# Kernel optimization log

Measured on AMD Instinct MI355X. Metric: run time of the kernel, lower is better.

Reference implementation:

```python
import jax, jax.numpy as jnp
import numpy as np
from jax import lax

T, B, D, H, C, G = 32, 512, 1024, 2048, 10, 16
BETA = 0.95
THRESH = 1.0


def _build_mask(key, out_f, in_f, p_intra=1.0, p_inter=0.15):
    ig, og = in_f // G, out_f // G
    same = (jnp.arange(out_f) // og)[:, None] == (jnp.arange(in_f) // ig)[None, :]
    probs = jnp.where(same, p_intra, p_inter)
    return (jax.random.uniform(key, (out_f, in_f)) < probs).astype(jnp.float32)


def setup_inputs() -> dict:
    key = jax.random.key(0)
    ks = jax.random.split(key, 12)
    def w(k, out_f, in_f):
        return jax.random.normal(k, (out_f, in_f), jnp.float32) * (1.0 / np.sqrt(in_f))
    return {
        'x_seq': jax.random.normal(ks[0], (T, B, D), jnp.float32),
        'w1': w(ks[1], H, D), 'b1': jax.random.normal(ks[2], (H,), jnp.float32) * 0.01,
        'mask1': _build_mask(ks[3], H, D),
        'w2': w(ks[4], H, H), 'b2': jax.random.normal(ks[5], (H,), jnp.float32) * 0.01,
        'mask2': _build_mask(ks[6], H, H),
        'w3': w(ks[7], H, H), 'b3': jax.random.normal(ks[8], (H,), jnp.float32) * 0.01,
        'mask3': _build_mask(ks[9], H, H),
        'w_out': w(ks[10], C, H), 'b_out': jax.random.normal(ks[11], (C,), jnp.float32) * 0.01,
    }


@jax.custom_vjp
def spike(x):
    # heaviside fire, fast_sigmoid(slope=25) surrogate gradient
    return (x > 0).astype(x.dtype)

def _spike_fwd(x):
    return spike(x), x

def _spike_bwd(x, g):
    return (g / (25.0 * jnp.abs(x) + 1.0) ** 2,)

spike.defvjp(_spike_fwd, _spike_bwd)


def _lif(cur, mem):
    # snntorch Leaky (reset-by-subtraction): reset from previous mem (detached)
    reset = lax.stop_gradient((mem > THRESH).astype(cur.dtype))
    mem = BETA * mem + cur - reset * THRESH
    spk = spike(mem - THRESH)
    return spk, mem


def reference(x_seq, w1, b1, mask1, w2, b2, mask2, w3, b3, mask3, w_out, b_out):
    # cache masked weights once (same math as per-step weight*mask)
    ew1, ew2, ew3 = w1 * mask1, w2 * mask2, w3 * mask3
    Bsz = x_seq.shape[1]
    mem1 = jnp.zeros((Bsz, H), x_seq.dtype)
    mem2 = jnp.zeros((Bsz, H), x_seq.dtype)
    mem3 = jnp.zeros((Bsz, H), x_seq.dtype)
    mem_o = jnp.zeros((Bsz, C), x_seq.dtype)
    ssum = jnp.zeros((Bsz, C), x_seq.dtype)

    def step(carry, x_t):
        mem1, mem2, mem3, mem_o, ssum = carry
        spk1, mem1 = _lif(x_t @ ew1.T + b1, mem1)
        spk2, mem2 = _lif(spk1 @ ew2.T + b2, mem2)
        spk3, mem3 = _lif(spk2 @ ew3.T + b3, mem3)
        spk_o, mem_o = _lif(spk3 @ w_out.T + b_out, mem_o)
        return (mem1, mem2, mem3, mem_o, ssum + spk_o), None

    (mem1, mem2, mem3, mem_o, ssum), _ = lax.scan(step, (mem1, mem2, mem3, mem_o, ssum), x_seq)
    return ssum
```

## Files before the change

kernel.cpp:

```cpp
#include <hip/hip_runtime.h>

#define TSTEPS 32
#define BSZ    512
#define DIN    1024
#define HID    2048
#define NCLS   10
#define BETA   0.95f
#define VTH    1.0f
#define SPKB   ((size_t)BSZ * (HID / 8))

typedef __attribute__((ext_vector_type(4))) float          f4;
typedef __attribute__((ext_vector_type(4))) float          f32x4;
typedef __attribute__((ext_vector_type(8))) __bf16         bf16x8;
typedef __attribute__((ext_vector_type(8))) unsigned short us8;
typedef __attribute__((ext_vector_type(4))) unsigned short us4;
typedef __attribute__((ext_vector_type(2))) unsigned int   u32x2;

__device__ inline unsigned short f2bf(float f) {
    unsigned u = __float_as_uint(f);
    u += 0x7FFF + ((u >> 16) & 1);
    return (unsigned short)(u >> 16);
}
__device__ inline float bf2f(unsigned short h) {
    return __uint_as_float(((unsigned)h) << 16);
}

__device__ __forceinline__ void split_f4pair(f4 v0, f4 v1, us8& o0, us8& o1, us8& o2) {
#pragma unroll
    for (int jj = 0; jj < 4; jj++) {
        float v = v0[jj];
        unsigned short h1 = f2bf(v); float r = v - bf2f(h1);
        unsigned short h2 = f2bf(r); float r2 = r - bf2f(h2);
        o0[jj] = h1; o1[jj] = h2; o2[jj] = f2bf(r2);
        v = v1[jj];
        h1 = f2bf(v); r = v - bf2f(h1);
        h2 = f2bf(r); r2 = r - bf2f(h2);
        o0[jj + 4] = h1; o1[jj + 4] = h2; o2[jj + 4] = f2bf(r2);
    }
}

__global__ __launch_bounds__(256)
void split3(const float* __restrict__ w, const float* __restrict__ m,
            unsigned short* __restrict__ h1, unsigned short* __restrict__ h2,
            unsigned short* __restrict__ h3, int n4)
{
    int i      = blockIdx.x * blockDim.x + threadIdx.x;
    int stride = gridDim.x * blockDim.x;
    for (; i < n4; i += stride) {
        f4 wv = ((const f4*)w)[i];
        f4 mv = ((const f4*)m)[i];
        us4 a, b, c;
#pragma unroll
        for (int j = 0; j < 4; j++) {
            float e  = wv[j] * mv[j];
            unsigned short x1 = f2bf(e);
            float r  = e - bf2f(x1);
            unsigned short x2 = f2bf(r);
            float r2 = r - bf2f(x2);
            a[j] = x1; b[j] = x2; c[j] = f2bf(r2);
        }
        ((us4*)h1)[i] = a;
        ((us4*)h2)[i] = b;
        ((us4*)h3)[i] = c;
    }
}

__global__ __launch_bounds__(256)
void split3q(const float* __restrict__ w, const float* __restrict__ m,
             unsigned short* __restrict__ q)
{
    const int NK = HID * HID;
    int gid = blockIdx.x * 256 + threadIdx.x;
    const int lane = gid & 63;
    const int t    = gid >> 6;
    const int kt   = t & (HID / 32 - 1);
    const int nt   = t >> 6;
    const int n = nt * 16 + (lane & 15);
    const int k = kt * 32 + (lane >> 4) * 8;
    const size_t src = (size_t)n * HID + k;
    f4 w0 = *(const f4*)(w + src),     w1v = *(const f4*)(w + src + 4);
    f4 m0 = *(const f4*)(m + src),     m1v = *(const f4*)(m + src + 4);
    us8 q0, q1, q2;
    split_f4pair(w0 * m0, w1v * m1v, q0, q1, q2);
    ((us8*)q)[gid]            = q0;
    ((us8*)(q + NK))[gid]     = q1;
    ((us8*)(q + 2 * NK))[gid] = q2;
}

__global__ __launch_bounds__(256)
void zerof(float* __restrict__ p, int n4)
{
    int i      = blockIdx.x * blockDim.x + threadIdx.x;
    int stride = gridDim.x * blockDim.x;
    f4 z = {0.f, 0.f, 0.f, 0.f};
    for (; i < n4; i += stride) ((f4*)p)[i] = z;
}

__device__ __forceinline__ void xsplit_dev(const float* __restrict__ xt,
                                           unsigned short* __restrict__ dst,
                                           int bid, int nblk, int tid)
{
    const int n4 = BSZ * DIN / 4;
    const int PS = BSZ * DIN;
    int i      = bid * 256 + tid;
    int stride = nblk * 256;
    for (; i < n4; i += stride) {
        f4 v = ((const f4*)xt)[i];
        us4 a, b, c;
#pragma unroll
        for (int j = 0; j < 4; j++) {
            float e = v[j];
            unsigned short x1 = f2bf(e);
            float r  = e - bf2f(x1);
            unsigned short x2 = f2bf(r);
            float r2 = r - bf2f(x2);
            a[j] = x1; b[j] = x2; c[j] = f2bf(r2);
        }
        ((us4*)(dst))[i]          = a;
        ((us4*)(dst + PS))[i]     = b;
        ((us4*)(dst + 2 * PS))[i] = c;
    }
}

__global__ __launch_bounds__(256)
void xsplit_k(const float* __restrict__ xt, unsigned short* __restrict__ dst)
{
    xsplit_dev(xt, dst, blockIdx.x, gridDim.x, threadIdx.x);
}

__device__ __forceinline__ void lif_epi(const f32x4 acc[2][2], const float* __restrict__ bias,
                                        float* __restrict__ memOut, unsigned char* __restrict__ sbits,
                                        int bm, int bn, int wm, int wn, int lane)
{
    const int fr = lane & 15;
#pragma unroll
    for (int fm = 0; fm < 2; fm++)
#pragma unroll
        for (int fn = 0; fn < 2; fn++) {
            const int n  = bn * 64 + wn * 32 + fn * 16 + fr;
            const float bv = bias[n];
            const int rbase = bm * 64 + wm * 32 + fm * 16 + (lane >> 4) * 4;
#pragma unroll
            for (int r = 0; r < 4; r++) {
                const int row = rbase + r;
                float* mp = memOut + (size_t)row * HID + n;
                float mo  = *mp;
                float m2  = BETA * mo + (acc[fm][fn][r] + bv) - ((mo > VTH) ? VTH : 0.f);
                *mp = m2;
                unsigned long long bal = __ballot(m2 > VTH);
                if (fr == 0) {
                    unsigned short bits = (unsigned short)(bal >> ((lane >> 4) * 16));
                    *(unsigned short*)(sbits + (size_t)row * (HID / 8) + bn * 8 + wn * 4 + fn * 2) = bits;
                }
            }
        }
}

__device__ __forceinline__ void lif_epi4b(const f32x4 (&acc)[4], const float* __restrict__ bias,
                                          float* __restrict__ memOut,
                                          unsigned char* __restrict__ sbitsOut,
                                          int bm, int bn, int wv, int lane)
{
    const int fr = lane & 15;
    const int n  = bn * 64 + wv * 16 + fr;
    const float bv = bias[n];
#pragma unroll
    for (int fm = 0; fm < 4; fm++) {
        const int rbase = bm * 64 + fm * 16 + (lane >> 4) * 4;
#pragma unroll
        for (int r = 0; r < 4; r++) {
            const int row = rbase + r;
            float* mp = memOut + (size_t)row * HID + n;
            float mo  = *mp;
            float m2  = BETA * mo + (acc[fm][r] + bv) - ((mo > VTH) ? VTH : 0.f);
            *mp = m2;
            unsigned long long bal = __ballot(m2 > VTH);
            if (fr == 0) {
                unsigned short bits = (unsigned short)(bal >> ((lane >> 4) * 16));
                *(unsigned short*)(sbitsOut + (size_t)row * (HID / 8) + bn * 8 + wv * 2) = bits;
            }
        }
    }
}

__device__ __forceinline__ void role_out_b(const unsigned char* __restrict__ sbits,
    const float* __restrict__ wo, const float* __restrict__ bo,
    float* __restrict__ memo, float* __restrict__ ssum, int b, int lane)
{
    const unsigned int bits = *(const unsigned int*)(sbits + (size_t)b * (HID / 8) + lane * 4);
    float acc[NCLS];
#pragma unroll
    for (int c = 0; c < NCLS; c++) {
        const f4* wrow = (const f4*)(wo + (size_t)c * HID + lane * 32);
        float s = 0.f;
#pragma unroll
        for (int q = 0; q < 8; q++) {
            f4 w = wrow[q];
#pragma unroll
            for (int i = 0; i < 4; i++)
                if ((bits >> (q * 4 + i)) & 1u) s += w[i];
        }
        acc[c] = s;
    }
#pragma unroll
    for (int c = 0; c < NCLS; c++)
#pragma unroll
        for (int m = 1; m < 64; m <<= 1) acc[c] += __shfl_xor(acc[c], m, 64);

    if (lane == 0) {
#pragma unroll
        for (int c = 0; c < NCLS; c++) {
            float mo  = memo[b * NCLS + c];
            float rst = (mo > VTH) ? VTH : 0.f;
            float m2  = BETA * mo + acc[c] + bo[c] - rst;
            memo[b * NCLS + c] = m2;
            if (m2 > VTH) ssum[b * NCLS + c] += 1.f;
        }
    }
}

__device__ __forceinline__ void role_l23b(unsigned char* smem,
    const unsigned char* __restrict__ sbitsIn,
    const unsigned short* __restrict__ Bp,
    const float* __restrict__ bias, float* __restrict__ memOut,
    unsigned char* __restrict__ sbitsOut, int rb, int tid)
{
    auto Bs = reinterpret_cast<unsigned short(*)[3][64 * 40]>(smem);
    const size_t PS = (size_t)HID * HID;

    const int bn = rb & 31, bm = rb >> 5;
    const int srow = tid >> 2, skq = tid & 3;
    const int lane = tid & 63, wv = tid >> 6;
    const int wm = wv >> 1, wn = wv & 1;
    const int fr = lane & 15, fk = (lane >> 4) * 8;
    const size_t bRow = (size_t)(bn * 64 + srow) * HID;
    const int sdst = srow * 40 + skq * 8;

    const unsigned char* aP0 = sbitsIn + (size_t)(bm * 64 + wm * 32 + fr) * (HID / 8);
    const unsigned char* aP1 = aP0 + (size_t)16 * (HID / 8);

    f32x4 acc[2][2] = {};
    us8 bb0, bb1, bb2;
    unsigned aw0, aw1;

    auto ldB = [&](int k0) {
        bb0 = *(const us8*)(Bp + bRow + k0 + skq * 8);
        bb1 = *(const us8*)(Bp + PS + bRow + k0 + skq * 8);
        bb2 = *(const us8*)(Bp + 2 * PS + bRow + k0 + skq * 8);
    };
    auto stage = [&](int nb) {
        *(us8*)&Bs[nb][0][sdst] = bb0;
        *(us8*)&Bs[nb][1][sdst] = bb1;
        *(us8*)&Bs[nb][2][sdst] = bb2;
    };

    ldB(0); stage(0);
    aw0 = *(const unsigned*)(aP0);
    aw1 = *(const unsigned*)(aP1);
    __syncthreads();

    const int nsteps = HID / 32;
    for (int s = 0; s < nsteps; s++) {
        const int buf = s & 1;
        const bool more = (s + 1 < nsteps);
        unsigned awn0 = 0, awn1 = 0;
        if (more) {
            ldB((s + 1) * 32);
            awn0 = *(const unsigned*)(aP0 + (s + 1) * 4);
            awn1 = *(const unsigned*)(aP1 + (s + 1) * 4);
        }

        bf16x8 af[2];
        {
            unsigned byt0 = aw0 >> fk, byt1 = aw1 >> fk;
            us8 e0, e1;
#pragma unroll
            for (int jj = 0; jj < 8; jj++) {
                e0[jj] = ((byt0 >> jj) & 1u) ? (unsigned short)0x3F80 : (unsigned short)0;
                e1[jj] = ((byt1 >> jj) & 1u) ? (unsigned short)0x3F80 : (unsigned short)0;
            }
            af[0] = *(bf16x8*)&e0;
            af[1] = *(bf16x8*)&e1;
        }

        bf16x8 bf[3][2];
#pragma unroll
        for (int fn = 0; fn < 2; fn++) {
            bf[0][fn] = *(const bf16x8*)&Bs[buf][0][(wn * 32 + fn * 16 + fr) * 40 + fk];
            bf[1][fn] = *(const bf16x8*)&Bs[buf][1][(wn * 32 + fn * 16 + fr) * 40 + fk];
            bf[2][fn] = *(const bf16x8*)&Bs[buf][2][(wn * 32 + fn * 16 + fr) * 40 + fk];
        }
#pragma unroll
        for (int fm = 0; fm < 2; fm++)
#pragma unroll
            for (int fn = 0; fn < 2; fn++) {
                acc[fm][fn] = __builtin_amdgcn_mfma_f32_16x16x32_bf16(af[fm], bf[0][fn], acc[fm][fn], 0, 0, 0);
                acc[fm][fn] = __builtin_amdgcn_mfma_f32_16x16x32_bf16(af[fm], bf[1][fn], acc[fm][fn], 0, 0, 0);
                acc[fm][fn] = __builtin_amdgcn_mfma_f32_16x16x32_bf16(af[fm], bf[2][fn], acc[fm][fn], 0, 0, 0);
            }

        if (more) { stage(buf ^ 1); aw0 = awn0; aw1 = awn1; }
        __syncthreads();
    }

    lif_epi(acc, bias, memOut, sbitsOut, bm, bn, wm, wn, lane);
}

__device__ __forceinline__ void role_l1p(unsigned char* smem,
    const unsigned short* __restrict__ Ap,
    const unsigned short* __restrict__ Wp,
    const float* __restrict__ bias, float* __restrict__ memOut,
    unsigned char* __restrict__ sbitsOut, int rb, int tid)
{
    auto As = reinterpret_cast<unsigned short(*)[64 * 40]>(smem);
    auto Bs = reinterpret_cast<unsigned short(*)[3][64 * 40]>(smem + 15360);
    const size_t APS = (size_t)BSZ * DIN;
    const size_t BPS = (size_t)HID * DIN;

    const int bn = rb & 31, bm = rb >> 5;
    const int srow = tid >> 2, skq = tid & 3;
    const int lane = tid & 63, wv = tid >> 6;
    const int wm = wv >> 1, wn = wv & 1;
    const int fr = lane & 15, fk = (lane >> 4) * 8;
    const size_t aRow = (size_t)(bm * 64 + srow) * DIN;
    const size_t bRow = (size_t)(bn * 64 + srow) * DIN;
    const int sdst = srow * 40 + skq * 8;

    f32x4 acc[2][2] = {};
    us8 aa0, aa1, aa2, bb0, bb1, bb2;

    auto ldnext = [&](int k0) {
        aa0 = *(const us8*)(Ap + aRow + k0 + skq * 8);
        aa1 = *(const us8*)(Ap + APS + aRow + k0 + skq * 8);
        aa2 = *(const us8*)(Ap + 2 * APS + aRow + k0 + skq * 8);
        bb0 = *(const us8*)(Wp + bRow + k0 + skq * 8);
        bb1 = *(const us8*)(Wp + BPS + bRow + k0 + skq * 8);
        bb2 = *(const us8*)(Wp + 2 * BPS + bRow + k0 + skq * 8);
    };
    auto stageA = [&]() {
        *(us8*)&As[0][sdst] = aa0;
        *(us8*)&As[1][sdst] = aa1;
        *(us8*)&As[2][sdst] = aa2;
    };
    auto stageB = [&](int nb) {
        *(us8*)&Bs[nb][0][sdst] = bb0;
        *(us8*)&Bs[nb][1][sdst] = bb1;
        *(us8*)&Bs[nb][2][sdst] = bb2;
    };

    ldnext(0); stageA(); stageB(0);
    __syncthreads();

    const int nsteps = DIN / 32;
    for (int s = 0; s < nsteps; s++) {
        const bool more = (s + 1 < nsteps);
        if (more) ldnext((s + 1) * 32);

        bf16x8 af[3][2], bf[3][2];
#pragma unroll
        for (int p = 0; p < 3; p++)
#pragma unroll
            for (int f = 0; f < 2; f++) {
                af[p][f] = *(const bf16x8*)&As[p][(wm * 32 + f * 16 + fr) * 40 + fk];
                bf[p][f] = *(const bf16x8*)&Bs[s & 1][p][(wn * 32 + f * 16 + fr) * 40 + fk];
            }
#pragma unroll
        for (int pa = 0; pa < 3; pa++)
#pragma unroll
            for (int pb = 0; pb < 3; pb++) {
                if (pa + pb <= 2) {
#pragma unroll
                    for (int fm = 0; fm < 2; fm++)
#pragma unroll
                        for (int fn = 0; fn < 2; fn++)
                            acc[fm][fn] = __builtin_amdgcn_mfma_f32_16x16x32_bf16(
                                af[pa][fm], bf[pb][fn], acc[fm][fn], 0, 0, 0);
                }
            }

        __syncthreads();
        if (more) { stageA(); stageB((s + 1) & 1); }
        __syncthreads();
    }

    lif_epi(acc, bias, memOut, sbitsOut, bm, bn, wm, wn, lane);
}

__global__ __launch_bounds__(256)
void snn_step2(const float* __restrict__ x,
               unsigned short* __restrict__ xp,
               const unsigned short* __restrict__ w1p, const float* __restrict__ b1,
               const unsigned short* __restrict__ w2p, const float* __restrict__ b2,
               const unsigned short* __restrict__ w3p, const float* __restrict__ b3,
               const float* __restrict__ wo, const float* __restrict__ bo,
               float* __restrict__ mem1, float* __restrict__ mem2, float* __restrict__ mem3,
               float* __restrict__ memo,
               unsigned char* __restrict__ spk1, unsigned char* __restrict__ spk2,
               unsigned char* __restrict__ spk3,
               float* __restrict__ ssum, int j)
{
    __shared__ __align__(16) unsigned char smem[46080];
    const int bid = blockIdx.x, tid = threadIdx.x;
    const size_t XSLOT = (size_t)3 * BSZ * DIN;

    if (bid < 256) {
        const int t = j;
        if (t <= TSTEPS - 1)
            role_l1p(smem, xp + (size_t)(t & 1) * XSLOT, w1p, b1, mem1,
                     spk1 + (size_t)(t & 1) * SPKB, bid, tid);
    } else if (bid < 512) {
        const int t = j - 1;
        if (t >= 0 && t <= TSTEPS - 1)
            role_l23b(smem, spk1 + (size_t)(t & 1) * SPKB, w2p, b2, mem2,
                      spk2 + (size_t)(t & 1) * SPKB, bid - 256, tid);
    } else if (bid < 768) {
        const int t = j - 2;
        if (t >= 0 && t <= TSTEPS - 1)
            role_l23b(smem, spk2 + (size_t)(t & 1) * SPKB, w3p, b3, mem3,
                      spk3 + (size_t)(t & 1) * SPKB, bid - 512, tid);
    } else {
        const int t1 = j + 1;
        if (t1 <= TSTEPS - 1)
            xsplit_dev(x + (size_t)t1 * BSZ * DIN,
                       xp + (size_t)(t1 & 1) * XSLOT, bid - 768, 128, tid);
        const int t = j - 3;
        if (t >= 0 && t <= TSTEPS - 1) {
            const int lane = tid & 63, wvi = tid >> 6;
            role_out_b(spk3 + (size_t)(t & 1) * SPKB, wo, bo, memo, ssum,
                       (bid - 768) * 4 + wvi, lane);
        }
    }
}


__device__ __forceinline__ void role_l23e(unsigned char* smem,
    const unsigned char* __restrict__ sbitsIn,
    const unsigned short* __restrict__ Bq,
    const float* __restrict__ bias, float* __restrict__ memOut,
    unsigned char* __restrict__ sbitsOut, int rb, int tid)
{
    u32x2* lut = (u32x2*)smem;
    if (tid < 16) {
        u32x2 e;
        e.x = ((tid & 1) ? 0x3F80u : 0u) | ((tid & 2) ? 0x3F800000u : 0u);
        e.y = ((tid & 4) ? 0x3F80u : 0u) | ((tid & 8) ? 0x3F800000u : 0u);
        lut[tid] = e;
    }
    __syncthreads();

    const int bn = rb & 31, bm = rb >> 5;
    const int lane = tid & 63, wv = tid >> 6;
    const int fr = lane & 15, fk = (lane >> 4) * 8;

    const size_t PSQ = (size_t)HID * HID / 8;
    const us8* bP0 = (const us8*)Bq + (size_t)(bn * 4 + wv) * (HID / 32) * 64 + lane;
    const us8* bP1 = bP0 + PSQ;
    const us8* bP2 = bP1 + PSQ;

    const unsigned char* aR = sbitsIn + (size_t)(bm * 64 + fr) * (HID / 8);

    f32x4 acc[4] = {};
    us8 bb[2][3];
    us4 awq[2][4];

#define LDB4(SET, S) do { const int sc_ = (S) < 64 ? (S) : 63;                 \
        bb[SET][0] = bP0[sc_ * 64];                                            \
        bb[SET][1] = bP1[sc_ * 64];                                            \
        bb[SET][2] = bP2[sc_ * 64]; } while (0)

#define LDA4(SET, G) do { const int gc_ = (G) < 16 ? (G) : 15;                 \
        awq[SET][0] = *(const us4*)(aR + 0 * 16 * (HID / 8) + gc_ * 16);       \
        awq[SET][1] = *(const us4*)(aR + 1 * 16 * (HID / 8) + gc_ * 16);       \
        awq[SET][2] = *(const us4*)(aR + 2 * 16 * (HID / 8) + gc_ * 16);       \
        awq[SET][3] = *(const us4*)(aR + 3 * 16 * (HID / 8) + gc_ * 16); } while (0)

#define EXPAND(AF, W) do { unsigned by_ = ((W) >> fk) & 0xFFu;                 \
        u32x2 lo_ = lut[by_ & 15u];                                            \
        u32x2 hi_ = lut[by_ >> 4];                                             \
        ((u32x2*)&(AF))[0] = lo_;                                              \
        ((u32x2*)&(AF))[1] = hi_; } while (0)

#define STEP(BSET, ASET, COMP) do {                                            \
        us8 a0_, a1_, a2_, a3_;                                                \
        EXPAND(a0_, awq[ASET][0][COMP]);                                       \
        EXPAND(a1_, awq[ASET][1][COMP]);                                       \
        EXPAND(a2_, awq[ASET][2][COMP]);                                       \
        EXPAND(a3_, awq[ASET][3][COMP]);                                       \
        bf16x8 b0_ = *(const bf16x8*)&bb[BSET][0];                             \
        bf16x8 b1_ = *(const bf16x8*)&bb[BSET][1];                             \
        bf16x8 b2_ = *(const bf16x8*)&bb[BSET][2];                             \
        bf16x8 fa0_ = *(const bf16x8*)&a0_;                                    \
        bf16x8 fa1_ = *(const bf16x8*)&a1_;                                    \
        bf16x8 fa2_ = *(const bf16x8*)&a2_;                                    \
        bf16x8 fa3_ = *(const bf16x8*)&a3_;                                    \
        acc[0] = __builtin_amdgcn_mfma_f32_16x16x32_bf16(fa0_, b0_, acc[0], 0, 0, 0); \
        acc[0] = __builtin_amdgcn_mfma_f32_16x16x32_bf16(fa0_, b1_, acc[0], 0, 0, 0); \
        acc[0] = __builtin_amdgcn_mfma_f32_16x16x32_bf16(fa0_, b2_, acc[0], 0, 0, 0); \
        acc[1] = __builtin_amdgcn_mfma_f32_16x16x32_bf16(fa1_, b0_, acc[1], 0, 0, 0); \
        acc[1] = __builtin_amdgcn_mfma_f32_16x16x32_bf16(fa1_, b1_, acc[1], 0, 0, 0); \
        acc[1] = __builtin_amdgcn_mfma_f32_16x16x32_bf16(fa1_, b2_, acc[1], 0, 0, 0); \
        acc[2] = __builtin_amdgcn_mfma_f32_16x16x32_bf16(fa2_, b0_, acc[2], 0, 0, 0); \
        acc[2] = __builtin_amdgcn_mfma_f32_16x16x32_bf16(fa2_, b1_, acc[2], 0, 0, 0); \
        acc[2] = __builtin_amdgcn_mfma_f32_16x16x32_bf16(fa2_, b2_, acc[2], 0, 0, 0); \
        acc[3] = __builtin_amdgcn_mfma_f32_16x16x32_bf16(fa3_, b0_, acc[3], 0, 0, 0); \
        acc[3] = __builtin_amdgcn_mfma_f32_16x16x32_bf16(fa3_, b1_, acc[3], 0, 0, 0); \
        acc[3] = __builtin_amdgcn_mfma_f32_16x16x32_bf16(fa3_, b2_, acc[3], 0, 0, 0); \
    } while (0)

    LDB4(0, 0); LDB4(1, 1);
    LDA4(0, 0); LDA4(1, 1);

    for (int g = 0; g < 16; g += 2) {
        const int s0 = g * 4;
        STEP(0, 0, 0); LDB4(0, s0 + 2);
        STEP(1, 0, 1); LDB4(1, s0 + 3);
        STEP(0, 0, 2); LDB4(0, s0 + 4);
        STEP(1, 0, 3); LDB4(1, s0 + 5);
        LDA4(0, g + 2);
        STEP(0, 1, 0); LDB4(0, s0 + 6);
        STEP(1, 1, 1); LDB4(1, s0 + 7);
        STEP(0, 1, 2); LDB4(0, s0 + 8);
        STEP(1, 1, 3); LDB4(1, s0 + 9);
        LDA4(1, g + 3);
    }

#undef LDB4
#undef LDA4
#undef EXPAND
#undef STEP

    lif_epi4b(acc, bias, memOut, sbitsOut, bm, bn, wv, lane);
}

__device__ __forceinline__ void role_l1s(unsigned char* smem,
    const unsigned short* __restrict__ Ap,
    const unsigned short* __restrict__ Wp,
    const float* __restrict__ bias, float* __restrict__ memOut,
    unsigned char* __restrict__ sbitsOut, int rb, int tid)
{
    auto As = reinterpret_cast<unsigned short(*)[64 * 40]>(smem);
    auto Bs = reinterpret_cast<unsigned short(*)[64 * 40]>(smem + 15360);
    const size_t APS = (size_t)BSZ * DIN;
    const size_t BPS = (size_t)HID * DIN;

    const int bn = rb & 31, bm = rb >> 5;
    const int srow = tid >> 2, skq = tid & 3;
    const int lane = tid & 63, wv = tid >> 6;
    const int wm = wv >> 1, wn = wv & 1;
    const int fr = lane & 15, fk = (lane >> 4) * 8;
    const size_t aRow = (size_t)(bm * 64 + srow) * DIN;
    const size_t bRow = (size_t)(bn * 64 + srow) * DIN;
    const int sdst = srow * 40 + skq * 8;

    f32x4 acc[2][2] = {};
    us8 aa0, aa1, aa2, bb0, bb1, bb2;

    auto ldnext = [&](int k0) {
        aa0 = *(const us8*)(Ap + aRow + k0 + skq * 8);
        aa1 = *(const us8*)(Ap + APS + aRow + k0 + skq * 8);
        aa2 = *(const us8*)(Ap + 2 * APS + aRow + k0 + skq * 8);
        bb0 = *(const us8*)(Wp + bRow + k0 + skq * 8);
        bb1 = *(const us8*)(Wp + BPS + bRow + k0 + skq * 8);
        bb2 = *(const us8*)(Wp + 2 * BPS + bRow + k0 + skq * 8);
    };
    auto stageAB = [&]() {
        *(us8*)&As[0][sdst] = aa0;
        *(us8*)&As[1][sdst] = aa1;
        *(us8*)&As[2][sdst] = aa2;
        *(us8*)&Bs[0][sdst] = bb0;
        *(us8*)&Bs[1][sdst] = bb1;
        *(us8*)&Bs[2][sdst] = bb2;
    };

    ldnext(0); stageAB();
    __syncthreads();

    const int nsteps = DIN / 32;
    for (int s = 0; s < nsteps; s++) {
        const bool more = (s + 1 < nsteps);
        if (more) ldnext((s + 1) * 32);

        bf16x8 af[3][2], bf[3][2];
#pragma unroll
        for (int p = 0; p < 3; p++)
#pragma unroll
            for (int f = 0; f < 2; f++) {
                af[p][f] = *(const bf16x8*)&As[p][(wm * 32 + f * 16 + fr) * 40 + fk];
                bf[p][f] = *(const bf16x8*)&Bs[p][(wn * 32 + f * 16 + fr) * 40 + fk];
            }
#pragma unroll
        for (int pa = 0; pa < 3; pa++)
#pragma unroll
            for (int pb = 0; pb < 3; pb++) {
                if (pa + pb <= 2) {
#pragma unroll
                    for (int fm = 0; fm < 2; fm++)
#pragma unroll
                        for (int fn = 0; fn < 2; fn++)
                            acc[fm][fn] = __builtin_amdgcn_mfma_f32_16x16x32_bf16(
                                af[pa][fm], bf[pb][fn], acc[fm][fn], 0, 0, 0);
                }
            }

        __syncthreads();
        if (more) stageAB();
        __syncthreads();
    }

    lif_epi(acc, bias, memOut, sbitsOut, bm, bn, wm, wn, lane);
}

__global__ __launch_bounds__(256, 4)
void snn_step4(const float* __restrict__ x,
               unsigned short* __restrict__ xp,
               const unsigned short* __restrict__ w1p, const float* __restrict__ b1,
               const unsigned short* __restrict__ w2q, const float* __restrict__ b2,
               const unsigned short* __restrict__ w3q, const float* __restrict__ b3,
               const float* __restrict__ wo, const float* __restrict__ bo,
               float* __restrict__ mem1, float* __restrict__ mem2, float* __restrict__ mem3,
               float* __restrict__ memo,
               unsigned char* __restrict__ spk1, unsigned char* __restrict__ spk2,
               unsigned char* __restrict__ spk3,
               float* __restrict__ ssum, int j)
{
    __shared__ __align__(16) unsigned char smem[30720];
    const int bid = blockIdx.x, tid = threadIdx.x;
    const size_t XSLOT = (size_t)3 * BSZ * DIN;

    if (bid < 256) {
        const int t = j;
        if (t <= TSTEPS - 1)
            role_l1s(smem, xp + (size_t)(t & 1) * XSLOT, w1p, b1, mem1,
                     spk1 + (size_t)(t & 1) * SPKB, bid, tid);
    } else if (bid < 512) {
        const int t = j - 1;
        if (t >= 0 && t <= TSTEPS - 1)
            role_l23e(smem, spk1 + (size_t)(t & 1) * SPKB, w2q, b2, mem2,
                      spk2 + (size_t)(t & 1) * SPKB, bid - 256, tid);
    } else if (bid < 768) {
        const int t = j - 2;
        if (t >= 0 && t <= TSTEPS - 1)
            role_l23e(smem, spk2 + (size_t)(t & 1) * SPKB, w3q, b3, mem3,
                      spk3 + (size_t)(t & 1) * SPKB, bid - 512, tid);
    } else {
        const int t1 = j + 1;
        if (t1 <= TSTEPS - 1)
            xsplit_dev(x + (size_t)t1 * BSZ * DIN,
                       xp + (size_t)(t1 & 1) * XSLOT, bid - 768, 256, tid);
        const int t = j - 3;
        if (t >= 0 && t <= TSTEPS - 1) {
            const int lane = tid & 63, wvi = tid >> 6;
            if (wvi < 2)
                role_out_b(spk3 + (size_t)(t & 1) * SPKB, wo, bo, memo, ssum,
                           (bid - 768) * 2 + wvi, lane);
        }
    }
}

extern "C" void kernel_launch(void* const* d_in, const int* in_sizes, int n_in,
                              void* d_out, int out_size, void* d_ws, size_t ws_size,
                              hipStream_t stream)
{
    const float* x  = (const float*)d_in[0];
    const float* w1 = (const float*)d_in[1];
    const float* b1 = (const float*)d_in[2];
    const float* m1 = (const float*)d_in[3];
    const float* w2 = (const float*)d_in[4];
    const float* b2 = (const float*)d_in[5];
    const float* m2 = (const float*)d_in[6];
    const float* w3 = (const float*)d_in[7];
    const float* b3 = (const float*)d_in[8];
    const float* m3 = (const float*)d_in[9];
    const float* wo = (const float*)d_in[10];
    const float* bo = (const float*)d_in[11];
    float* out = (float*)d_out;

    const size_t planeB  = (size_t)HID * HID * 2;
    const size_t plane1B = (size_t)HID * DIN * 2;
    const size_t planeXB = (size_t)BSZ * DIN * 2;
    const size_t memB    = (size_t)BSZ * HID * 4;
    const size_t memoB   = (size_t)BSZ * NCLS * 4;
    const size_t spk2B   = 2 * SPKB;

    unsigned char* base = (unsigned char*)d_ws;

    const size_t needV4 = 6 * planeB + 3 * plane1B + 6 * planeXB
                        + 3 * memB + memoB + 3 * spk2B + 4096;

    const int nW1  = HID * DIN / 4;
    const size_t HH = (size_t)HID * HID;
    const size_t HD = (size_t)HID * DIN;

    if (ws_size >= needV4) {
        unsigned short* w2q = (unsigned short*)base;
        unsigned short* w3q = (unsigned short*)(base + 3 * planeB);
        unsigned short* w1p = (unsigned short*)(base + 6 * planeB);
        unsigned short* xp  = (unsigned short*)(base + 6 * planeB + 3 * plane1B);
        unsigned char* mbase = base + 6 * planeB + 3 * plane1B + 6 * planeXB;
        float* mem1 = (float*)(mbase);
        float* mem2 = (float*)(mbase + memB);
        float* mem3 = (float*)(mbase + 2 * memB);
        float* memo = (float*)(mbase + 3 * memB);
        unsigned char* spk1 = mbase + 3 * memB + memoB;
        unsigned char* spk2 = spk1 + spk2B;
        unsigned char* spk3 = spk2 + spk2B;

        split3q<<<2048, 256, 0, stream>>>(w2, m2, w2q);
        split3q<<<2048, 256, 0, stream>>>(w3, m3, w3q);
        split3<<<1024, 256, 0, stream>>>(w1, m1, w1p, w1p + HD, w1p + 2 * HD, nW1);
        xsplit_k<<<256, 256, 0, stream>>>(x, xp);

        zerof<<<1024, 256, 0, stream>>>(mem1, (int)((3 * memB + memoB) / 16));
        zerof<<<8, 256, 0, stream>>>(out, (BSZ * NCLS) / 4);

        for (int j = 0; j <= TSTEPS + 2; j++) {
            snn_step4<<<1024, 256, 0, stream>>>(x, xp, w1p, b1, w2q, b2, w3q, b3,
                                                wo, bo, mem1, mem2, mem3, memo,
                                                spk1, spk2, spk3, out, j);
        }
        return;
    }

    const size_t needV2 = 6 * planeB + 3 * plane1B + 6 * planeXB
                        + 3 * memB + memoB + 3 * spk2B;
    if (ws_size < needV2) return;

    unsigned short* w2p = (unsigned short*)base;
    unsigned short* w3p = (unsigned short*)(base + 3 * planeB);
    unsigned short* w1p = (unsigned short*)(base + 6 * planeB);
    unsigned short* xp  = (unsigned short*)(base + 6 * planeB + 3 * plane1B);
    unsigned char* mbase = base + 6 * planeB + 3 * plane1B + 6 * planeXB;
    float* mem1 = (float*)(mbase);
    float* mem2 = (float*)(mbase + memB);
    float* mem3 = (float*)(mbase + 2 * memB);
    float* memo = (float*)(mbase + 3 * memB);
    unsigned char* spk1 = mbase + 3 * memB + memoB;
    unsigned char* spk2 = spk1 + spk2B;
    unsigned char* spk3 = spk2 + spk2B;

    const int nW23 = HID * HID / 4;
    split3<<<1024, 256, 0, stream>>>(w2, m2, w2p, w2p + HH, w2p + 2 * HH, nW23);
    split3<<<1024, 256, 0, stream>>>(w3, m3, w3p, w3p + HH, w3p + 2 * HH, nW23);
    split3<<<1024, 256, 0, stream>>>(w1, m1, w1p, w1p + HD, w1p + 2 * HD, nW1);
    xsplit_k<<<256, 256, 0, stream>>>(x, xp);

    zerof<<<1024, 256, 0, stream>>>(mem1, (int)((3 * memB + memoB) / 16));
    zerof<<<8, 256, 0, stream>>>(out, (BSZ * NCLS) / 4);

    for (int j = 0; j <= TSTEPS + 2; j++) {
        snn_step2<<<896, 256, 0, stream>>>(x, xp, w1p, b1, w2p, b2, w3p, b3,
                                           wo, bo, mem1, mem2, mem3, memo,
                                           spk1, spk2, spk3, out, j);
    }
}
```

Baseline: 1.738 ms.

## Split hidden-layer GEMMs into K-halves across a deeper wavefront pipeline

Replaces the step4 pipeline with step7, which splits each hidden-layer GEMM (layers 2 and 3) into two K-halves handled by separate block groups in consecutive launches. Partial sums go through global buffers, and spike buffers are triple-buffered so the deeper schedule stays correct. Layer 1 now reads the input split directly from an MFMA-fragment-ordered layout (new xsplitq) instead of staging it through LDS. The aim is to cut per-launch critical-path latency and raise occupancy with more, shorter blocks, at the cost of two extra pipeline stages, partial-sum global traffic, and more launches.

```diff
diff --git a/kernel.cpp b/kernel.cpp
--- a/kernel.cpp
+++ b/kernel.cpp
@@ -128,6 +128,35 @@
     xsplit_dev(xt, dst, blockIdx.x, gridDim.x, threadIdx.x);
 }
 
+__device__ __forceinline__ void xsplitq_dev(const float* __restrict__ xt,
+                                            unsigned short* __restrict__ dstu,
+                                            int bid, int tid)
+{
+    us8* dst = (us8*)dstu;
+    const int gid  = bid * 256 + tid;
+    const int lane = gid & 63;
+    const int t2   = gid >> 6;
+    const int kt   = t2 & 31;
+    const int rt   = t2 >> 5;
+    const int n = rt * 16 + (lane & 15);
+    const int k = kt * 32 + (lane >> 4) * 8;
+    const size_t src = (size_t)n * DIN + k;
+    f4 v0 = *(const f4*)(xt + src);
+    f4 v1 = *(const f4*)(xt + src + 4);
+    us8 q0, q1, q2;
+    split_f4pair(v0, v1, q0, q1, q2);
+    const size_t XPS = (size_t)BSZ * DIN / 8;
+    dst[gid]            = q0;
+    dst[XPS + gid]      = q1;
+    dst[2 * XPS + gid]  = q2;
+}
+
+__global__ __launch_bounds__(256)
+void xsplitq_k(const float* __restrict__ xt, unsigned short* __restrict__ dst)
+{
+    xsplitq_dev(xt, dst, blockIdx.x, threadIdx.x);
+}
+
 __device__ __forceinline__ void lif_epi(const f32x4 acc[2][2], const float* __restrict__ bias,
                                         float* __restrict__ memOut, unsigned char* __restrict__ sbits,
                                         int bm, int bn, int wm, int wn, int lane)
@@ -218,220 +247,6 @@
         }
     }
 }
-
-__device__ __forceinline__ void role_l23b(unsigned char* smem,
-    const unsigned char* __restrict__ sbitsIn,
-    const unsigned short* __restrict__ Bp,
-    const float* __restrict__ bias, float* __restrict__ memOut,
-    unsigned char* __restrict__ sbitsOut, int rb, int tid)
-{
-    auto Bs = reinterpret_cast<unsigned short(*)[3][64 * 40]>(smem);
-    const size_t PS = (size_t)HID * HID;
-
-    const int bn = rb & 31, bm = rb >> 5;
-    const int srow = tid >> 2, skq = tid & 3;
-    const int lane = tid & 63, wv = tid >> 6;
-    const int wm = wv >> 1, wn = wv & 1;
-    const int fr = lane & 15, fk = (lane >> 4) * 8;
-    const size_t bRow = (size_t)(bn * 64 + srow) * HID;
-    const int sdst = srow * 40 + skq * 8;
-
-    const unsigned char* aP0 = sbitsIn + (size_t)(bm * 64 + wm * 32 + fr) * (HID / 8);
-    const unsigned char* aP1 = aP0 + (size_t)16 * (HID / 8);
-
-    f32x4 acc[2][2] = {};
-    us8 bb0, bb1, bb2;
-    unsigned aw0, aw1;
-
-    auto ldB = [&](int k0) {
-        bb0 = *(const us8*)(Bp + bRow + k0 + skq * 8);
-        bb1 = *(const us8*)(Bp + PS + bRow + k0 + skq * 8);
-        bb2 = *(const us8*)(Bp + 2 * PS + bRow + k0 + skq * 8);
-    };
-    auto stage = [&](int nb) {
-        *(us8*)&Bs[nb][0][sdst] = bb0;
-        *(us8*)&Bs[nb][1][sdst] = bb1;
-        *(us8*)&Bs[nb][2][sdst] = bb2;
-    };
-
-    ldB(0); stage(0);
-    aw0 = *(const unsigned*)(aP0);
-    aw1 = *(const unsigned*)(aP1);
-    __syncthreads();
-
-    const int nsteps = HID / 32;
-    for (int s = 0; s < nsteps; s++) {
-        const int buf = s & 1;
-        const bool more = (s + 1 < nsteps);
-        unsigned awn0 = 0, awn1 = 0;
-        if (more) {
-            ldB((s + 1) * 32);
-            awn0 = *(const unsigned*)(aP0 + (s + 1) * 4);
-            awn1 = *(const unsigned*)(aP1 + (s + 1) * 4);
-        }
-
-        bf16x8 af[2];
-        {
-            unsigned byt0 = aw0 >> fk, byt1 = aw1 >> fk;
-            us8 e0, e1;
-#pragma unroll
-            for (int jj = 0; jj < 8; jj++) {
-                e0[jj] = ((byt0 >> jj) & 1u) ? (unsigned short)0x3F80 : (unsigned short)0;
-                e1[jj] = ((byt1 >> jj) & 1u) ? (unsigned short)0x3F80 : (unsigned short)0;
-            }
-            af[0] = *(bf16x8*)&e0;
-            af[1] = *(bf16x8*)&e1;
-        }
-
-        bf16x8 bf[3][2];
-#pragma unroll
-        for (int fn = 0; fn < 2; fn++) {
-            bf[0][fn] = *(const bf16x8*)&Bs[buf][0][(wn * 32 + fn * 16 + fr) * 40 + fk];
-            bf[1][fn] = *(const bf16x8*)&Bs[buf][1][(wn * 32 + fn * 16 + fr) * 40 + fk];
-            bf[2][fn] = *(const bf16x8*)&Bs[buf][2][(wn * 32 + fn * 16 + fr) * 40 + fk];
-        }
-#pragma unroll
-        for (int fm = 0; fm < 2; fm++)
-#pragma unroll
-            for (int fn = 0; fn < 2; fn++) {
-                acc[fm][fn] = __builtin_amdgcn_mfma_f32_16x16x32_bf16(af[fm], bf[0][fn], acc[fm][fn], 0, 0, 0);
-                acc[fm][fn] = __builtin_amdgcn_mfma_f32_16x16x32_bf16(af[fm], bf[1][fn], acc[fm][fn], 0, 0, 0);
-                acc[fm][fn] = __builtin_amdgcn_mfma_f32_16x16x32_bf16(af[fm], bf[2][fn], acc[fm][fn], 0, 0, 0);
-            }
-
-        if (more) { stage(buf ^ 1); aw0 = awn0; aw1 = awn1; }
-        __syncthreads();
-    }
-
-    lif_epi(acc, bias, memOut, sbitsOut, bm, bn, wm, wn, lane);
-}
-
-__device__ __forceinline__ void role_l1p(unsigned char* smem,
-    const unsigned short* __restrict__ Ap,
-    const unsigned short* __restrict__ Wp,
-    const float* __restrict__ bias, float* __restrict__ memOut,
-    unsigned char* __restrict__ sbitsOut, int rb, int tid)
-{
-    auto As = reinterpret_cast<unsigned short(*)[64 * 40]>(smem);
-    auto Bs = reinterpret_cast<unsigned short(*)[3][64 * 40]>(smem + 15360);
-    const size_t APS = (size_t)BSZ * DIN;
-    const size_t BPS = (size_t)HID * DIN;
-
-    const int bn = rb & 31, bm = rb >> 5;
-    const int srow = tid >> 2, skq = tid & 3;
-    const int lane = tid & 63, wv = tid >> 6;
-    const int wm = wv >> 1, wn = wv & 1;
-    const int fr = lane & 15, fk = (lane >> 4) * 8;
-    const size_t aRow = (size_t)(bm * 64 + srow) * DIN;
-    const size_t bRow = (size_t)(bn * 64 + srow) * DIN;
-    const int sdst = srow * 40 + skq * 8;
-
-    f32x4 acc[2][2] = {};
-    us8 aa0, aa1, aa2, bb0, bb1, bb2;
-
-    auto ldnext = [&](int k0) {
-        aa0 = *(const us8*)(Ap + aRow + k0 + skq * 8);
-        aa1 = *(const us8*)(Ap + APS + aRow + k0 + skq * 8);
-        aa2 = *(const us8*)(Ap + 2 * APS + aRow + k0 + skq * 8);
-        bb0 = *(const us8*)(Wp + bRow + k0 + skq * 8);
-        bb1 = *(const us8*)(Wp + BPS + bRow + k0 + skq * 8);
-        bb2 = *(const us8*)(Wp + 2 * BPS + bRow + k0 + skq * 8);
-    };
-    auto stageA = [&]() {
-        *(us8*)&As[0][sdst] = aa0;
-        *(us8*)&As[1][sdst] = aa1;
-        *(us8*)&As[2][sdst] = aa2;
-    };
-    auto stageB = [&](int nb) {
-        *(us8*)&Bs[nb][0][sdst] = bb0;
-        *(us8*)&Bs[nb][1][sdst] = bb1;
-        *(us8*)&Bs[nb][2][sdst] = bb2;
-    };
-
-    ldnext(0); stageA(); stageB(0);
-    __syncthreads();
-
-    const int nsteps = DIN / 32;
-    for (int s = 0; s < nsteps; s++) {
-        const bool more = (s + 1 < nsteps);
-        if (more) ldnext((s + 1) * 32);
-
-        bf16x8 af[3][2], bf[3][2];
-#pragma unroll
-        for (int p = 0; p < 3; p++)
-#pragma unroll
-            for (int f = 0; f < 2; f++) {
-                af[p][f] = *(const bf16x8*)&As[p][(wm * 32 + f * 16 + fr) * 40 + fk];
-                bf[p][f] = *(const bf16x8*)&Bs[s & 1][p][(wn * 32 + f * 16 + fr) * 40 + fk];
-            }
-#pragma unroll
-        for (int pa = 0; pa < 3; pa++)
-#pragma unroll
-            for (int pb = 0; pb < 3; pb++) {
-                if (pa + pb <= 2) {
-#pragma unroll
-                    for (int fm = 0; fm < 2; fm++)
-#pragma unroll
-                        for (int fn = 0; fn < 2; fn++)
-                            acc[fm][fn] = __builtin_amdgcn_mfma_f32_16x16x32_bf16(
-                                af[pa][fm], bf[pb][fn], acc[fm][fn], 0, 0, 0);
-                }
-            }
-
-        __syncthreads();
-        if (more) { stageA(); stageB((s + 1) & 1); }
-        __syncthreads();
-    }
-
-    lif_epi(acc, bias, memOut, sbitsOut, bm, bn, wm, wn, lane);
-}
-
-__global__ __launch_bounds__(256)
-void snn_step2(const float* __restrict__ x,
-               unsigned short* __restrict__ xp,
-               const unsigned short* __restrict__ w1p, const float* __restrict__ b1,
-               const unsigned short* __restrict__ w2p, const float* __restrict__ b2,
-               const unsigned short* __restrict__ w3p, const float* __restrict__ b3,
-               const float* __restrict__ wo, const float* __restrict__ bo,
-               float* __restrict__ mem1, float* __restrict__ mem2, float* __restrict__ mem3,
-               float* __restrict__ memo,
-               unsigned char* __restrict__ spk1, unsigned char* __restrict__ spk2,
-               unsigned char* __restrict__ spk3,
-               float* __restrict__ ssum, int j)
-{
-    __shared__ __align__(16) unsigned char smem[46080];
-    const int bid = blockIdx.x, tid = threadIdx.x;
-    const size_t XSLOT = (size_t)3 * BSZ * DIN;
-
-    if (bid < 256) {
-        const int t = j;
-        if (t <= TSTEPS - 1)
-            role_l1p(smem, xp + (size_t)(t & 1) * XSLOT, w1p, b1, mem1,
-                     spk1 + (size_t)(t & 1) * SPKB, bid, tid);
-    } else if (bid < 512) {
-        const int t = j - 1;
-        if (t >= 0 && t <= TSTEPS - 1)
-            role_l23b(smem, spk1 + (size_t)(t & 1) * SPKB, w2p, b2, mem2,
-                      spk2 + (size_t)(t & 1) * SPKB, bid - 256, tid);
-    } else if (bid < 768) {
-        const int t = j - 2;
-        if (t >= 0 && t <= TSTEPS - 1)
-            role_l23b(smem, spk2 + (size_t)(t & 1) * SPKB, w3p, b3, mem3,
-                      spk3 + (size_t)(t & 1) * SPKB, bid - 512, tid);
-    } else {
-        const int t1 = j + 1;
-        if (t1 <= TSTEPS - 1)
-            xsplit_dev(x + (size_t)t1 * BSZ * DIN,
-                       xp + (size_t)(t1 & 1) * XSLOT, bid - 768, 128, tid);
-        const int t = j - 3;
-        if (t >= 0 && t <= TSTEPS - 1) {
-            const int lane = tid & 63, wvi = tid >> 6;
-            role_out_b(spk3 + (size_t)(t & 1) * SPKB, wo, bo, memo, ssum,
-                       (bid - 768) * 4 + wvi, lane);
-        }
-    }
-}
-
 
 __device__ __forceinline__ void role_l23e(unsigned char* smem,
     const unsigned char* __restrict__ sbitsIn,
@@ -657,6 +472,273 @@
     }
 }
 
+
+__device__ __forceinline__ void role_l1f(unsigned char* smem,
+    const unsigned short* __restrict__ xq,
+    const unsigned short* __restrict__ Wp,
+    const float* __restrict__ bias, float* __restrict__ memOut,
+    unsigned char* __restrict__ sbitsOut, int rb, int tid)
+{
+    auto Bs = reinterpret_cast<unsigned short(*)[64 * 40]>(smem);
+    const size_t BPS = (size_t)HID * DIN;
+    const size_t XPS = (size_t)BSZ * DIN / 8;
+    const us8* xq8 = (const us8*)xq;
+
+    const int bn = rb & 31, bm = rb >> 5;
+    const int srow = tid >> 2, skq = tid & 3;
+    const int lane = tid & 63, wvv = tid >> 6;
+    const int wm = wvv >> 1, wn = wvv & 1;
+    const int fr = lane & 15, fk = (lane >> 4) * 8;
+    const size_t bRow = (size_t)(bn * 64 + srow) * DIN;
+    const int sdst = srow * 40 + skq * 8;
+    const int rt0 = bm * 4 + wm * 2;
+
+    f32x4 acc[2][2] = {};
+    us8 bb0, bb1, bb2;
+
+    auto ldB = [&](int k0) {
+        bb0 = *(const us8*)(Wp + bRow + k0 + skq * 8);
+        bb1 = *(const us8*)(Wp + BPS + bRow + k0 + skq * 8);
+        bb2 = *(const us8*)(Wp + 2 * BPS + bRow + k0 + skq * 8);
+    };
+    auto stageB = [&]() {
+        *(us8*)&Bs[0][sdst] = bb0;
+        *(us8*)&Bs[1][sdst] = bb1;
+        *(us8*)&Bs[2][sdst] = bb2;
+    };
+
+    ldB(0); stageB();
+    __syncthreads();
+
+    const int nsteps = DIN / 32;
+    for (int s = 0; s < nsteps; s++) {
+        const bool more = (s + 1 < nsteps);
+        if (more) ldB((s + 1) * 32);
+
+        us8 axr[3][2];
+#pragma unroll
+        for (int p = 0; p < 3; p++)
+#pragma unroll
+            for (int f = 0; f < 2; f++)
+                axr[p][f] = xq8[(size_t)p * XPS + (size_t)((rt0 + f) * 32 + s) * 64 + lane];
+
+        bf16x8 bf[3][2];
+#pragma unroll
+        for (int p = 0; p < 3; p++)
+#pragma unroll
+            for (int f = 0; f < 2; f++)
+                bf[p][f] = *(const bf16x8*)&Bs[p][(wn * 32 + f * 16 + fr) * 40 + fk];
+
+#pragma unroll
+        for (int pa = 0; pa < 3; pa++)
+#pragma unroll
+            for (int pb = 0; pb < 3; pb++) {
+                if (pa + pb <= 2) {
+#pragma unroll
+                    for (int fm = 0; fm < 2; fm++)
+#pragma unroll
+                        for (int fn = 0; fn < 2; fn++)
+                            acc[fm][fn] = __builtin_amdgcn_mfma_f32_16x16x32_bf16(
+                                *(const bf16x8*)&axr[pa][fm], bf[pb][fn], acc[fm][fn], 0, 0, 0);
+                }
+            }
+
+        __syncthreads();
+        if (more) stageB();
+        __syncthreads();
+    }
+
+    lif_epi(acc, bias, memOut, sbitsOut, bm, bn, wm, wn, lane);
+}
+
+template<int HALF>
+__device__ __forceinline__ void role_l23h(unsigned char* smem,
+    const unsigned char* __restrict__ sbitsIn,
+    const unsigned short* __restrict__ Bq,
+    float* __restrict__ partial,
+    const float* __restrict__ bias, float* __restrict__ memOut,
+    unsigned char* __restrict__ sbitsOut, int rb, int tid)
+{
+    u32x2* lut = (u32x2*)smem;
+    if (tid < 16) {
+        u32x2 e;
+        e.x = ((tid & 1) ? 0x3F80u : 0u) | ((tid & 2) ? 0x3F800000u : 0u);
+        e.y = ((tid & 4) ? 0x3F80u : 0u) | ((tid & 8) ? 0x3F800000u : 0u);
+        lut[tid] = e;
+    }
+    __syncthreads();
+
+    const int bn = rb & 31, bm = rb >> 5;
+    const int lane = tid & 63, wv = tid >> 6;
+    const int fr = lane & 15, fk = (lane >> 4) * 8;
+
+    const size_t PSQ = (size_t)HID * HID / 8;
+    const us8* bP0 = (const us8*)Bq + (size_t)(bn * 4 + wv) * (HID / 32) * 64 + lane;
+    const us8* bP1 = bP0 + PSQ;
+    const us8* bP2 = bP1 + PSQ;
+
+    const unsigned char* aR = sbitsIn + (size_t)(bm * 64 + fr) * (HID / 8);
+
+    float* pB = partial + (size_t)(rb * 4 + wv) * 1024 + lane * 4;
+
+    f32x4 acc[4];
+    if (HALF == 0) {
+        acc[0] = f32x4{0.f, 0.f, 0.f, 0.f};
+        acc[1] = f32x4{0.f, 0.f, 0.f, 0.f};
+        acc[2] = f32x4{0.f, 0.f, 0.f, 0.f};
+        acc[3] = f32x4{0.f, 0.f, 0.f, 0.f};
+    } else {
+        acc[0] = *(const f32x4*)(pB + 0 * 256);
+        acc[1] = *(const f32x4*)(pB + 1 * 256);
+        acc[2] = *(const f32x4*)(pB + 2 * 256);
+        acc[3] = *(const f32x4*)(pB + 3 * 256);
+    }
+
+    us8 bb[2][3];
+    us4 awq[2][4];
+
+#define LDB4(SET, S) do { const int sc_ = (S) < 64 ? (S) : 63;                 \
+        bb[SET][0] = bP0[sc_ * 64];                                            \
+        bb[SET][1] = bP1[sc_ * 64];                                            \
+        bb[SET][2] = bP2[sc_ * 64]; } while (0)
+
+#define LDA4(SET, G) do { const int gc_ = (G) < 16 ? (G) : 15;                 \
+        awq[SET][0] = *(const us4*)(aR + 0 * 16 * (HID / 8) + gc_ * 16);       \
+        awq[SET][1] = *(const us4*)(aR + 1 * 16 * (HID / 8) + gc_ * 16);       \
+        awq[SET][2] = *(const us4*)(aR + 2 * 16 * (HID / 8) + gc_ * 16);       \
+        awq[SET][3] = *(const us4*)(aR + 3 * 16 * (HID / 8) + gc_ * 16); } while (0)
+
+#define EXPAND(AF, W) do { unsigned by_ = ((W) >> fk) & 0xFFu;                 \
+        u32x2 lo_ = lut[by_ & 15u];                                            \
+        u32x2 hi_ = lut[by_ >> 4];                                             \
+        ((u32x2*)&(AF))[0] = lo_;                                              \
+        ((u32x2*)&(AF))[1] = hi_; } while (0)
+
+#define STEP(BSET, ASET, COMP) do {                                            \
+        us8 a0_, a1_, a2_, a3_;                                                \
+        EXPAND(a0_, awq[ASET][0][COMP]);                                       \
+        EXPAND(a1_, awq[ASET][1][COMP]);                                       \
+        EXPAND(a2_, awq[ASET][2][COMP]);                                       \
+        EXPAND(a3_, awq[ASET][3][COMP]);                                       \
+        bf16x8 b0_ = *(const bf16x8*)&bb[BSET][0];                             \
+        bf16x8 b1_ = *(const bf16x8*)&bb[BSET][1];                             \
+        bf16x8 b2_ = *(const bf16x8*)&bb[BSET][2];                             \
+        bf16x8 fa0_ = *(const bf16x8*)&a0_;                                    \
+        bf16x8 fa1_ = *(const bf16x8*)&a1_;                                    \
+        bf16x8 fa2_ = *(const bf16x8*)&a2_;                                    \
+        bf16x8 fa3_ = *(const bf16x8*)&a3_;                                    \
+        acc[0] = __builtin_amdgcn_mfma_f32_16x16x32_bf16(fa0_, b0_, acc[0], 0, 0, 0); \
+        acc[0] = __builtin_amdgcn_mfma_f32_16x16x32_bf16(fa0_, b1_, acc[0], 0, 0, 0); \
+        acc[0] = __builtin_amdgcn_mfma_f32_16x16x32_bf16(fa0_, b2_, acc[0], 0, 0, 0); \
+        acc[1] = __builtin_amdgcn_mfma_f32_16x16x32_bf16(fa1_, b0_, acc[1], 0, 0, 0); \
+        acc[1] = __builtin_amdgcn_mfma_f32_16x16x32_bf16(fa1_, b1_, acc[1], 0, 0, 0); \
+        acc[1] = __builtin_amdgcn_mfma_f32_16x16x32_bf16(fa1_, b2_, acc[1], 0, 0, 0); \
+        acc[2] = __builtin_amdgcn_mfma_f32_16x16x32_bf16(fa2_, b0_, acc[2], 0, 0, 0); \
+        acc[2] = __builtin_amdgcn_mfma_f32_16x16x32_bf16(fa2_, b1_, acc[2], 0, 0, 0); \
+        acc[2] = __builtin_amdgcn_mfma_f32_16x16x32_bf16(fa2_, b2_, acc[2], 0, 0, 0); \
+        acc[3] = __builtin_amdgcn_mfma_f32_16x16x32_bf16(fa3_, b0_, acc[3], 0, 0, 0); \
+        acc[3] = __builtin_amdgcn_mfma_f32_16x16x32_bf16(fa3_, b1_, acc[3], 0, 0, 0); \
+        acc[3] = __builtin_amdgcn_mfma_f32_16x16x32_bf16(fa3_, b2_, acc[3], 0, 0, 0); \
+    } while (0)
+
+    constexpr int S0 = HALF * 32;
+    constexpr int G0 = HALF * 8;
+
+    LDB4(0, S0); LDB4(1, S0 + 1);
+    LDA4(0, G0); LDA4(1, G0 + 1);
+
+    for (int g = G0; g < G0 + 8; g += 2) {
+        const int s0 = g * 4;
+        STEP(0, 0, 0); LDB4(0, s0 + 2);
+        STEP(1, 0, 1); LDB4(1, s0 + 3);
+        STEP(0, 0, 2); LDB4(0, s0 + 4);
+        STEP(1, 0, 3); LDB4(1, s0 + 5);
+        LDA4(0, g + 2);
+        STEP(0, 1, 0); LDB4(0, s0 + 6);
+        STEP(1, 1, 1); LDB4(1, s0 + 7);
+        STEP(0, 1, 2); LDB4(0, s0 + 8);
+        STEP(1, 1, 3); LDB4(1, s0 + 9);
+        LDA4(1, g + 3);
+    }
+
+#undef LDB4
+#undef LDA4
+#undef EXPAND
+#undef STEP
+
+    if (HALF == 0) {
+        *(f32x4*)(pB + 0 * 256) = acc[0];
+        *(f32x4*)(pB + 1 * 256) = acc[1];
+        *(f32x4*)(pB + 2 * 256) = acc[2];
+        *(f32x4*)(pB + 3 * 256) = acc[3];
+    } else {
+        lif_epi4b(acc, bias, memOut, sbitsOut, bm, bn, wv, lane);
+    }
+}
+
+__global__ __launch_bounds__(256, 6)
+void snn_step7(const float* __restrict__ x,
+               unsigned short* __restrict__ xq,
+               const unsigned short* __restrict__ w1p, const float* __restrict__ b1,
+               const unsigned short* __restrict__ w2q, const float* __restrict__ b2,
+               const unsigned short* __restrict__ w3q, const float* __restrict__ b3,
+               const float* __restrict__ wo, const float* __restrict__ bo,
+               float* __restrict__ mem1, float* __restrict__ mem2, float* __restrict__ mem3,
+               float* __restrict__ memo,
+               unsigned char* __restrict__ spk1, unsigned char* __restrict__ spk2,
+               unsigned char* __restrict__ spk3,
+               float* __restrict__ p2, float* __restrict__ p3,
+               float* __restrict__ ssum, int j)
+{
+    __shared__ __align__(16) unsigned char smem[15360];
+    const int bid = blockIdx.x, tid = threadIdx.x;
+    const size_t XSLOT = (size_t)3 * BSZ * DIN;
+    const size_t PHALF = (size_t)BSZ * HID;
+
+    if (bid < 256) {
+        const int t = j;
+        if (t <= TSTEPS - 1)
+            role_l1f(smem, xq + (size_t)(t & 1) * XSLOT, w1p, b1, mem1,
+                     spk1 + (size_t)(t % 3) * SPKB, bid, tid);
+    } else if (bid < 512) {
+        const int t = j - 1;
+        if (t >= 0 && t <= TSTEPS - 1)
+            role_l23h<0>(smem, spk1 + (size_t)(t % 3) * SPKB, w2q,
+                         p2 + (size_t)(t & 1) * PHALF,
+                         nullptr, nullptr, nullptr, bid - 256, tid);
+    } else if (bid < 768) {
+        const int t = j - 2;
+        if (t >= 0 && t <= TSTEPS - 1)
+            role_l23h<1>(smem, spk1 + (size_t)(t % 3) * SPKB, w2q,
+                         p2 + (size_t)(t & 1) * PHALF,
+                         b2, mem2, spk2 + (size_t)(t % 3) * SPKB, bid - 512, tid);
+    } else if (bid < 1024) {
+        const int t = j - 3;
+        if (t >= 0 && t <= TSTEPS - 1)
+            role_l23h<0>(smem, spk2 + (size_t)(t % 3) * SPKB, w3q,
+                         p3 + (size_t)(t & 1) * PHALF,
+                         nullptr, nullptr, nullptr, bid - 768, tid);
+    } else if (bid < 1280) {
+        const int t = j - 4;
+        if (t >= 0 && t <= TSTEPS - 1)
+            role_l23h<1>(smem, spk2 + (size_t)(t % 3) * SPKB, w3q,
+                         p3 + (size_t)(t & 1) * PHALF,
+                         b3, mem3, spk3 + (size_t)(t & 1) * SPKB, bid - 1024, tid);
+    } else {
+        const int t1 = j + 1;
+        if (t1 <= TSTEPS - 1)
+            xsplitq_dev(x + (size_t)t1 * BSZ * DIN,
+                        xq + (size_t)(t1 & 1) * XSLOT, bid - 1280, tid);
+        const int t = j - 5;
+        if (t >= 0 && t <= TSTEPS - 1) {
+            const int lane = tid & 63, wvi = tid >> 6;
+            if (wvi < 2)
+                role_out_b(spk3 + (size_t)(t & 1) * SPKB, wo, bo, memo, ssum,
+                           (bid - 1280) * 2 + wvi, lane);
+        }
+    }
+}
+
 extern "C" void kernel_launch(void* const* d_in, const int* in_sizes, int n_in,
                               void* d_out, int out_size, void* d_ws, size_t ws_size,
                               hipStream_t stream)
@@ -680,53 +762,49 @@
     const size_t planeXB = (size_t)BSZ * DIN * 2;
     const size_t memB    = (size_t)BSZ * HID * 4;
     const size_t memoB   = (size_t)BSZ * NCLS * 4;
-    const size_t spk2B   = 2 * SPKB;
+    const size_t partB   = (size_t)BSZ * HID * 4;
 
     unsigned char* base = (unsigned char*)d_ws;
-
-    const size_t needV4 = 6 * planeB + 3 * plane1B + 6 * planeXB
-                        + 3 * memB + memoB + 3 * spk2B + 4096;
-
     const int nW1  = HID * DIN / 4;
-    const size_t HH = (size_t)HID * HID;
     const size_t HD = (size_t)HID * DIN;
 
-    if (ws_size >= needV4) {
+    const size_t needV7 = 6 * planeB + 3 * plane1B + 6 * planeXB
+                        + 3 * memB + memoB + 8 * SPKB + 4 * partB + 4096;
+
+    if (ws_size >= needV7) {
         unsigned short* w2q = (unsigned short*)base;
         unsigned short* w3q = (unsigned short*)(base + 3 * planeB);
         unsigned short* w1p = (unsigned short*)(base + 6 * planeB);
-        unsigned short* xp  = (unsigned short*)(base + 6 * planeB + 3 * plane1B);
+        unsigned short* xq  = (unsigned short*)(base + 6 * planeB + 3 * plane1B);
         unsigned char* mbase = base + 6 * planeB + 3 * plane1B + 6 * planeXB;
         float* mem1 = (float*)(mbase);
         float* mem2 = (float*)(mbase + memB);
         float* mem3 = (float*)(mbase + 2 * memB);
         float* memo = (float*)(mbase + 3 * memB);
         unsigned char* spk1 = mbase + 3 * memB + memoB;
-        unsigned char* spk2 = spk1 + spk2B;
-        unsigned char* spk3 = spk2 + spk2B;
+        unsigned char* spk2 = spk1 + 3 * SPKB;
+        unsigned char* spk3 = spk2 + 3 * SPKB;
+        float* p2 = (float*)(spk3 + 2 * SPKB);
+        float* p3 = (float*)((unsigned char*)p2 + 2 * partB);
 
         split3q<<<2048, 256, 0, stream>>>(w2, m2, w2q);
         split3q<<<2048, 256, 0, stream>>>(w3, m3, w3q);
         split3<<<1024, 256, 0, stream>>>(w1, m1, w1p, w1p + HD, w1p + 2 * HD, nW1);
-        xsplit_k<<<256, 256, 0, stream>>>(x, xp);
+        xsplitq_k<<<256, 256, 0, stream>>>(x, xq);
 
         zerof<<<1024, 256, 0, stream>>>(mem1, (int)((3 * memB + memoB) / 16));
         zerof<<<8, 256, 0, stream>>>(out, (BSZ * NCLS) / 4);
 
-        for (int j = 0; j <= TSTEPS + 2; j++) {
-            snn_step4<<<1024, 256, 0, stream>>>(x, xp, w1p, b1, w2q, b2, w3q, b3,
+        for (int j = 0; j <= TSTEPS + 4; j++) {
+            snn_step7<<<1536, 256, 0, stream>>>(x, xq, w1p, b1, w2q, b2, w3q, b3,
                                                 wo, bo, mem1, mem2, mem3, memo,
-                                                spk1, spk2, spk3, out, j);
+                                                spk1, spk2, spk3, p2, p3, out, j);
         }
         return;
     }
 
-    const size_t needV2 = 6 * planeB + 3 * plane1B + 6 * planeXB
-                        + 3 * memB + memoB + 3 * spk2B;
-    if (ws_size < needV2) return;
-
-    unsigned short* w2p = (unsigned short*)base;
-    unsigned short* w3p = (unsigned short*)(base + 3 * planeB);
+    unsigned short* w2q = (unsigned short*)base;
+    unsigned short* w3q = (unsigned short*)(base + 3 * planeB);
     unsigned short* w1p = (unsigned short*)(base + 6 * planeB);
     unsigned short* xp  = (unsigned short*)(base + 6 * planeB + 3 * plane1B);
     unsigned char* mbase = base + 6 * planeB + 3 * plane1B + 6 * planeXB;
@@ -735,12 +813,11 @@
     float* mem3 = (float*)(mbase + 2 * memB);
     float* memo = (float*)(mbase + 3 * memB);
     unsigned char* spk1 = mbase + 3 * memB + memoB;
-    unsigned char* spk2 = spk1 + spk2B;
-    unsigned char* spk3 = spk2 + spk2B;
-
-    const int nW23 = HID * HID / 4;
-    split3<<<1024, 256, 0, stream>>>(w2, m2, w2p, w2p + HH, w2p + 2 * HH, nW23);
-    split3<<<1024, 256, 0, stream>>>(w3, m3, w3p, w3p + HH, w3p + 2 * HH, nW23);
+    unsigned char* spk2 = spk1 + 2 * SPKB;
+    unsigned char* spk3 = spk2 + 2 * SPKB;
+
+    split3q<<<2048, 256, 0, stream>>>(w2, m2, w2q);
+    split3q<<<2048, 256, 0, stream>>>(w3, m3, w3q);
     split3<<<1024, 256, 0, stream>>>(w1, m1, w1p, w1p + HD, w1p + 2 * HD, nW1);
     xsplit_k<<<256, 256, 0, stream>>>(x, xp);
 
@@ -748,8 +825,8 @@
     zerof<<<8, 256, 0, stream>>>(out, (BSZ * NCLS) / 4);
 
     for (int j = 0; j <= TSTEPS + 2; j++) {
-        snn_step2<<<896, 256, 0, stream>>>(x, xp, w1p, b1, w2p, b2, w3p, b3,
-                                           wo, bo, mem1, mem2, mem3, memo,
-                                           spk1, spk2, spk3, out, j);
-    }
-}
+        snn_step4<<<1024, 256, 0, stream>>>(x, xp, w1p, b1, w2q, b2, w3q, b3,
+                                            wo, bo, mem1, mem2, mem3, memo,
+                                            spk1, spk2, spk3, out, j);
+    }
+}
```

Result: slower. 1.983 ms (+14.1%).
